# Optimization experiments

Measured on AMD Instinct MI355X. Metric: run time of the kernel, lower is better.

## Reference

```python
import jax, jax.numpy as jnp
import numpy as np

H, KV, D = 12, 4, 128  # n_head, n_kv_head, head_dim
VE_GATE_CH = 12

def _rmsnorm(x):
    eps = jnp.finfo(x.dtype).eps  # matches torch F.rms_norm default eps
    return x * jax.lax.rsqrt(jnp.mean(x * x, axis=-1, keepdims=True) + eps)

def _rope(x, cos, sin):
    d = x.shape[-1] // 2
    x1, x2 = x[..., :d], x[..., d:]
    return jnp.concatenate([x1 * cos + x2 * sin, -x1 * sin + x2 * cos], axis=-1)

def setup_inputs() -> dict:
    key = jax.random.key(0)
    ks = jax.random.split(key, 9)
    B, T, C = 2, 2048, 1536
    x = jax.random.normal(ks[0], (B, T, C), jnp.float32)
    ve = jax.random.normal(ks[1], (B, T, KV * D), jnp.float32)
    ang = jax.random.uniform(ks[2], (1, T, 1, D // 2), jnp.float32) * (2.0 * np.pi)
    cos, sin = jnp.cos(ang), jnp.sin(ang)
    Wq = jax.random.normal(ks[3], (H * D, C), jnp.float32) * 0.02
    Wk = jax.random.normal(ks[4], (KV * D, C), jnp.float32) * 0.02
    Wv = jax.random.normal(ks[5], (KV * D, C), jnp.float32) * 0.02
    Wproj = jax.random.normal(ks[6], (C, C), jnp.float32) * 0.02
    Wg = jax.random.normal(ks[7], (KV, VE_GATE_CH), jnp.float32) * 0.02
    return dict(x=x, ve=ve, cos=cos, sin=sin, Wq=Wq, Wk=Wk, Wv=Wv, Wproj=Wproj, Wg=Wg, window=1024)

def reference(x, ve, cos, sin, Wq, Wk, Wv, Wproj, Wg, window):
    B, T, C = x.shape
    q = (x @ Wq.T).reshape(B, T, H, D)
    k = (x @ Wk.T).reshape(B, T, KV, D)
    v = (x @ Wv.T).reshape(B, T, KV, D)
    # value-embedding gate: 3*sigmoid(Linear(x[..., :12])) per kv head
    gate = 3.0 * jax.nn.sigmoid(x[..., :VE_GATE_CH] @ Wg.T)  # [B,T,KV]
    v = v + gate[..., None] * ve.reshape(B, T, KV, D)
    q = _rmsnorm(_rope(q, cos, sin)) * 1.2
    k = _rmsnorm(_rope(k, cos, sin)) * 1.2
    rep = H // KV  # GQA group size
    qh = q.transpose(0, 2, 1, 3).reshape(B, KV, rep, T, D)
    kh = k.transpose(0, 2, 1, 3)  # [B,KV,T,D]
    vh = v.transpose(0, 2, 1, 3)
    scores = jnp.einsum('bgrtd,bgsd->bgrts', qh, kh) / np.sqrt(D)
    row = jnp.arange(T)[:, None]
    col = jnp.arange(T)[None, :]
    if window < 0 or window >= T:
        mask = col <= row  # pure causal
    else:
        mask = (col <= row) & (row - col <= window)  # causal sliding window
    scores = jnp.where(mask, scores, -jnp.inf)
    att = jax.nn.softmax(scores, axis=-1)
    y = jnp.einsum('bgrts,bgsd->bgrtd', att, vh)
    y = y.reshape(B, H, T, D).transpose(0, 2, 1, 3).reshape(B, T, H * D)
    return y @ Wproj.T
```

## Files before the change

kernel.cpp:

```cpp
#include <hip/hip_runtime.h>
#include <hip/hip_bf16.h>
#include <math.h>

#define B_  2
#define T_  2048
#define C_  1536
#define H_  12
#define KV_ 4
#define D_  128
#define M_  (B_*T_)
#define REP_ (H_/KV_)
#define NQKV_ 2560

typedef __bf16 bf16x8 __attribute__((ext_vector_type(8)));
typedef float  f32x4  __attribute__((ext_vector_type(4)));
typedef unsigned u32x4 __attribute__((ext_vector_type(4)));

union BCast { u32x4 u; bf16x8 b; };

__device__ inline bf16x8 ldb8(const ushort* p) {
    BCast c; c.u = *reinterpret_cast<const u32x4*>(p); return c.b;
}

__device__ inline ushort f2bf(float f) {
    union { float f; unsigned u; } v; v.f = f;
    unsigned u = v.u;
    return (ushort)((u + 0x7FFF + ((u >> 16) & 1)) >> 16);
}

__device__ inline float bf2f(ushort u) {
    union { unsigned u; float f; } v; v.u = (unsigned)u << 16;
    return v.f;
}

__device__ inline void async_copy16(const ushort* g, ushort* l) {
    __builtin_amdgcn_global_load_lds(
        (const __attribute__((address_space(1))) unsigned*)g,
        (__attribute__((address_space(3))) unsigned*)l, 16, 0, 0);
}

__device__ __host__ inline int dperm(int d) {
    return (d < 32) ? d : (d < 64 ? d + 32 : (d < 96 ? d - 32 : d));
}

template<bool BF16OUT>
__global__ __launch_bounds__(256) void gemm_bf16_bt(const ushort* __restrict__ A,
                                                    const ushort* __restrict__ Bm,
                                                    void* __restrict__ Cp,
                                                    int M, int N, int K) {
    __shared__ ushort As[128 * 32];
    __shared__ ushort Bs[128 * 32];
    const int tid  = threadIdx.x;
    const int wave = tid >> 6, lane = tid & 63;
    const int m16 = lane & 15, quad = lane >> 4;
    const int bm = blockIdx.y * 128, bn = blockIdx.x * 128;
    const int wm = (wave >> 1) * 64, wn = (wave & 1) * 64;

    const int lrow = lane >> 2;
    const int lcol = (lane & 3) * 8;
    const ushort* Ag = A  + (size_t)(bm + wave * 16 + lrow) * K + lcol;
    const ushort* Bg = Bm + (size_t)(bn + wave * 16 + lrow) * K + lcol;
    ushort* AsW0 = As + wave * 512;
    ushort* AsW1 = As + 2048 + wave * 512;
    ushort* BsW0 = Bs + wave * 512;
    ushort* BsW1 = Bs + 2048 + wave * 512;
    const size_t rowskip = (size_t)64 * K;

    f32x4 acc[4][4];
    #pragma unroll
    for (int i = 0; i < 4; i++)
        #pragma unroll
        for (int j = 0; j < 4; j++) acc[i][j] = (f32x4){0.f, 0.f, 0.f, 0.f};

    for (int k0 = 0; k0 < K; k0 += 32) {
        async_copy16(Ag + k0,           AsW0);
        async_copy16(Ag + k0 + rowskip, AsW1);
        async_copy16(Bg + k0,           BsW0);
        async_copy16(Bg + k0 + rowskip, BsW1);
        __syncthreads();

        bf16x8 af[4], bfr[4];
        #pragma unroll
        for (int i = 0; i < 4; i++)
            af[i] = ldb8(As + (wm + i * 16 + m16) * 32 + quad * 8);
        #pragma unroll
        for (int j = 0; j < 4; j++)
            bfr[j] = ldb8(Bs + (wn + j * 16 + m16) * 32 + quad * 8);
        #pragma unroll
        for (int i = 0; i < 4; i++)
            #pragma unroll
            for (int j = 0; j < 4; j++)
                acc[i][j] = __builtin_amdgcn_mfma_f32_16x16x32_bf16(af[i], bfr[j], acc[i][j], 0, 0, 0);
        __syncthreads();
    }

    #pragma unroll
    for (int i = 0; i < 4; i++) {
        #pragma unroll
        for (int reg = 0; reg < 4; reg++) {
            const int row = bm + wm + i * 16 + quad * 4 + reg;
            if constexpr (BF16OUT) {
                ushort* C = (ushort*)Cp;
                #pragma unroll
                for (int j = 0; j < 4; j++)
                    C[(size_t)row * N + bn + wn + j * 16 + m16] = f2bf(acc[i][j][reg]);
            } else {
                float* C = (float*)Cp;
                #pragma unroll
                for (int j = 0; j < 4; j++)
                    C[(size_t)row * N + bn + wn + j * 16 + m16] = acc[i][j][reg];
            }
        }
    }
}

#define KQ_ 1536
__global__ __launch_bounds__(256) void gemm_qkv(const ushort* __restrict__ A,
                                                const ushort* __restrict__ Bm,
                                                ushort* __restrict__ Qp,
                                                ushort* __restrict__ Kp,
                                                ushort* __restrict__ vbuf,
                                                const float* __restrict__ cosb,
                                                const float* __restrict__ sinb) {
    __shared__ ushort As[128 * 32];
    __shared__ ushort Bs[128 * 32];
    const int tid  = threadIdx.x;
    const int wave = tid >> 6, lane = tid & 63;
    const int m16 = lane & 15, quad = lane >> 4;
    const int bm = blockIdx.y * 128, bn = blockIdx.x * 128;
    const int wm = (wave >> 1) * 64, wn = (wave & 1) * 64;

    const int lrow = lane >> 2;
    const int lcol = (lane & 3) * 8;
    const ushort* Ag = A  + (size_t)(bm + wave * 16 + lrow) * KQ_ + lcol;
    const ushort* Bg = Bm + (size_t)(bn + wave * 16 + lrow) * KQ_ + lcol;
    ushort* AsW0 = As + wave * 512;
    ushort* AsW1 = As + 2048 + wave * 512;
    ushort* BsW0 = Bs + wave * 512;
    ushort* BsW1 = Bs + 2048 + wave * 512;
    const size_t rowskip = (size_t)64 * KQ_;

    f32x4 acc[4][4];
    #pragma unroll
    for (int i = 0; i < 4; i++)
        #pragma unroll
        for (int j = 0; j < 4; j++) acc[i][j] = (f32x4){0.f, 0.f, 0.f, 0.f};

    for (int k0 = 0; k0 < KQ_; k0 += 32) {
        async_copy16(Ag + k0,           AsW0);
        async_copy16(Ag + k0 + rowskip, AsW1);
        async_copy16(Bg + k0,           BsW0);
        async_copy16(Bg + k0 + rowskip, BsW1);
        __syncthreads();

        bf16x8 af[4], bfr[4];
        #pragma unroll
        for (int i = 0; i < 4; i++)
            af[i] = ldb8(As + (wm + i * 16 + m16) * 32 + quad * 8);
        #pragma unroll
        for (int j = 0; j < 4; j++)
            bfr[j] = ldb8(Bs + (wn + j * 16 + m16) * 32 + quad * 8);
        #pragma unroll
        for (int i = 0; i < 4; i++)
            #pragma unroll
            for (int j = 0; j < 4; j++)
                acc[i][j] = __builtin_amdgcn_mfma_f32_16x16x32_bf16(af[i], bfr[j], acc[i][j], 0, 0, 0);
        __syncthreads();
    }

    if (bn < 2048) {
        float* ssqS = (float*)As;
        float ssq[4][4];
        #pragma unroll
        for (int i = 0; i < 4; i++) {
            #pragma unroll
            for (int reg = 0; reg < 4; reg++) {
                float v = acc[i][0][reg]*acc[i][0][reg] + acc[i][1][reg]*acc[i][1][reg]
                        + acc[i][2][reg]*acc[i][2][reg] + acc[i][3][reg]*acc[i][3][reg];
                v += __shfl_xor(v, 1); v += __shfl_xor(v, 2);
                v += __shfl_xor(v, 4); v += __shfl_xor(v, 8);
                ssq[i][reg] = v;
            }
        }
        if (m16 == 0) {
            #pragma unroll
            for (int i = 0; i < 4; i++)
                #pragma unroll
                for (int reg = 0; reg < 4; reg++)
                    ssqS[(wm + i*16 + quad*4 + reg) * 2 + (wave & 1)] = ssq[i][reg];
        }
        __syncthreads();

        const bool isq = (bn < 1536);
        const float osc = isq ? (1.2f * 1.2f * 0.08838834764831845f) : 1.0f;
        const int hh  = isq ? (bn >> 7) : ((bn - 1536) >> 7);
        const int nh  = isq ? H_ : KV_;
        ushort* outp  = isq ? Qp : Kp;

        float scl[4][4];
        #pragma unroll
        for (int i = 0; i < 4; i++) {
            #pragma unroll
            for (int reg = 0; reg < 4; reg++) {
                const int r = wm + i*16 + quad*4 + reg;
                const float tot = ssqS[r*2] + ssqS[r*2 + 1];
                scl[i][reg] = rsqrtf(tot * (1.0f/128.0f) + 1.1920928955078125e-07f) * osc;
            }
        }

        #pragma unroll
        for (int i = 0; i < 4; i++) {
            #pragma unroll
            for (int reg = 0; reg < 4; reg++) {
                const int row = bm + wm + i*16 + quad*4 + reg;
                const int b = row >> 11, t = row & (T_ - 1);
                ushort* orow = outp + ((size_t)(b * nh + hh) * T_ + t) * D_;
                const float sc = scl[i][reg];
                #pragma unroll
                for (int jp = 0; jp < 2; jp++) {
                    const int ipair = (wn ? 32 : 0) + jp*16 + m16;
                    const float c = cosb[t*64 + ipair], s = sinb[t*64 + ipair];
                    const float x1 = acc[i][jp][reg], x2 = acc[i][jp+2][reg];
                    orow[wn + jp*16 + m16]       = f2bf((x1*c + x2*s) * sc);
                    orow[wn + (jp+2)*16 + m16]   = f2bf((x2*c - x1*s) * sc);
                }
            }
        }
    } else {
        const int cb = bn - 2048 + wn;
        #pragma unroll
        for (int i = 0; i < 4; i++) {
            #pragma unroll
            for (int reg = 0; reg < 4; reg++) {
                const int row = bm + wm + i*16 + quad*4 + reg;
                ushort* vr = vbuf + (size_t)row * 512 + cb + m16;
                #pragma unroll
                for (int j = 0; j < 4; j++)
                    vr[j*16] = f2bf(acc[i][j][reg]);
            }
        }
    }
}

#define SEG0 1572864
#define SEG1 2162688
#define SEG2 2359296
#define SEG3 2555904
#define SEG4 3145728
#define ROW4 384
__global__ __launch_bounds__(256) void cast_all(const float* __restrict__ x,
                                                const float* __restrict__ Wq,
                                                const float* __restrict__ Wk,
                                                const float* __restrict__ Wv,
                                                const float* __restrict__ Wp,
                                                ushort* __restrict__ xb,
                                                ushort* __restrict__ Wqkvb,
                                                ushort* __restrict__ Wpb) {
    const int i = blockIdx.x * 256 + threadIdx.x;
    float4 v; size_t dst4; ushort* dstp;
    if (i < SEG0) {
        v = ((const float4*)x)[i]; dstp = xb; dst4 = i;
    } else if (i < SEG1) {
        const int j = i - SEG0;
        const int r = j / ROW4, c4 = j - r * ROW4;
        const int d = r & 127, hh = r >> 7;
        v = ((const float4*)Wq)[j]; dstp = Wqkvb;
        dst4 = (size_t)(hh * 128 + dperm(d)) * ROW4 + c4;
    } else if (i < SEG2) {
        const int j = i - SEG1;
        const int r = j / ROW4, c4 = j - r * ROW4;
        const int d = r & 127, g = r >> 7;
        v = ((const float4*)Wk)[j]; dstp = Wqkvb;
        dst4 = (size_t)(1536 + g * 128 + dperm(d)) * ROW4 + c4;
    } else if (i < SEG3) {
        const int j = i - SEG2;
        v = ((const float4*)Wv)[j]; dstp = Wqkvb;
        dst4 = (size_t)2048 * ROW4 + j;
    } else {
        const int j = i - SEG3;
        v = ((const float4*)Wp)[j]; dstp = Wpb; dst4 = j;
    }
    ((ushort4*)dstp)[dst4] = make_ushort4(f2bf(v.x), f2bf(v.y), f2bf(v.z), f2bf(v.w));
}

__global__ __launch_bounds__(256) void gate_vt(const ushort* __restrict__ vbuf,
                                               const float* __restrict__ x,
                                               const float* __restrict__ ve,
                                               const float* __restrict__ Wg,
                                               ushort* __restrict__ Vt) {
    const int t0 = blockIdx.x * 64, g = blockIdx.y, b = blockIdx.z;
    __shared__ float gateS[64];
    __shared__ ushort tile[128][66];
    const int tid = threadIdx.x;
    if (tid < 64) {
        const float* xr = x + (size_t)(b * T_ + t0 + tid) * C_;
        float acc = 0.f;
        #pragma unroll
        for (int c = 0; c < 12; c++) acc += xr[c] * Wg[g * 12 + c];
        gateS[tid] = 3.0f / (1.0f + __expf(-acc));
    }
    __syncthreads();
    #pragma unroll
    for (int i = 0; i < 32; i++) {
        int idx = i * 256 + tid;
        int r = idx >> 7;
        int d = idx & 127;
        size_t offv = (size_t)(b * T_ + t0 + r) * 512 + g * D_ + d;
        tile[d][r] = f2bf(bf2f(vbuf[offv]) + gateS[r] * ve[offv]);
    }
    __syncthreads();
    ushort* ob = Vt + ((size_t)(b * KV_ + g) * D_) * T_ + t0;
    #pragma unroll
    for (int i = 0; i < 32; i++) {
        int idx = i * 256 + tid;
        int d = idx >> 6;
        int c = idx & 63;
        ob[(size_t)d * T_ + c] = tile[d][c];
    }
}

__global__ __launch_bounds__(256, 3) void attn_mfma(const ushort* __restrict__ Qp,
                                                    const ushort* __restrict__ Kp,
                                                    const ushort* __restrict__ Vt,
                                                    ushort* __restrict__ Y,
                                                    const int* __restrict__ wptr) {
    const int t0 = blockIdx.x * 64;
    const int h  = blockIdx.y, b = blockIdx.z;
    const int g  = h / REP_;
    const int tid  = threadIdx.x;
    const int wave = tid >> 6, lane = tid & 63;
    const int m16 = lane & 15, quad = lane >> 4;

    __shared__ ushort Ks[4 * 32 * 32];
    __shared__ ushort Vs[128 * 32];
    __shared__ ushort Pl[4][16 * 40];

    const int w = *wptr;
    const bool windowed = (w >= 0 && w < T_);
    const unsigned wu = windowed ? (unsigned)w : 0x7FFFFFFFu;
    int s_lo = 0;
    if (windowed) { s_lo = t0 - w; if (s_lo < 0) s_lo = 0; }
    const int s_hi = t0 + 63;
    const int ss0 = s_lo & ~31;
    const int tw = t0 + wave * 16;

    const ushort* qrow = Qp + ((size_t)(b * H_ + h) * T_ + tw + m16) * D_ + quad * 8;
    bf16x8 qa[4];
    #pragma unroll
    for (int kc = 0; kc < 4; kc++) qa[kc] = ldb8(qrow + kc * 32);

    const ushort* kbase = Kp + (size_t)(b * KV_ + g) * T_ * D_;
    const ushort* vbase = Vt + (size_t)(b * KV_ + g) * D_ * T_;

    const int c0 = wave, c1 = wave + 4;
    const ushort* kg0 = kbase + (size_t)((c0 & 1) * 16 + (lane >> 2)) * D_ + (c0 >> 1) * 32 + (lane & 3) * 8;
    const ushort* kg1 = kbase + (size_t)((c1 & 1) * 16 + (lane >> 2)) * D_ + (c1 >> 1) * 32 + (lane & 3) * 8;
    ushort* kl0 = Ks + c0 * 512;
    ushort* kl1 = Ks + c1 * 512;
    const ushort* vg0 = vbase + (size_t)(c0 * 16 + (lane >> 2)) * T_ + (lane & 3) * 8;
    const ushort* vg1 = vbase + (size_t)(c1 * 16 + (lane >> 2)) * T_ + (lane & 3) * 8;
    ushort* vl0 = Vs + c0 * 512;
    ushort* vl1 = Vs + c1 * 512;

    f32x4 o[8];
    #pragma unroll
    for (int dt = 0; dt < 8; dt++) o[dt] = (f32x4){0.f, 0.f, 0.f, 0.f};
    f32x4 lacc = (f32x4){0.f, 0.f, 0.f, 0.f};
    BCast onesc; onesc.u = (u32x4){0x3F803F80u, 0x3F803F80u, 0x3F803F80u, 0x3F803F80u};
    const bf16x8 ones = onesc.b;
    ushort* pw = &Pl[wave][0];

    for (int ss = ss0; ss <= s_hi; ss += 32) {
        const size_t koff = (size_t)ss * D_;
        async_copy16(kg0 + koff, kl0);
        async_copy16(kg1 + koff, kl1);
        async_copy16(vg0 + ss,   vl0);
        async_copy16(vg1 + ss,   vl1);
        __syncthreads();

        f32x4 s0 = (f32x4){0.f,0.f,0.f,0.f};
        f32x4 s1 = (f32x4){0.f,0.f,0.f,0.f};
        #pragma unroll
        for (int kc = 0; kc < 4; kc++) {
            bf16x8 kf0 = ldb8(Ks + kc * 1024 + m16 * 32 + quad * 8);
            bf16x8 kf1 = ldb8(Ks + kc * 1024 + (16 + m16) * 32 + quad * 8);
            s0 = __builtin_amdgcn_mfma_f32_16x16x32_bf16(qa[kc], kf0, s0, 0, 0, 0);
            s1 = __builtin_amdgcn_mfma_f32_16x16x32_bf16(qa[kc], kf1, s1, 0, 0, 0);
        }

        const int sA = ss + m16, sB = ss + 16 + m16;
        #pragma unroll
        for (int reg = 0; reg < 4; reg++) {
            const int t = tw + quad * 4 + reg;
            const float pa = ((unsigned)(t - sA) <= wu) ? __expf(s0[reg]) : 0.f;
            const float pb = ((unsigned)(t - sB) <= wu) ? __expf(s1[reg]) : 0.f;
            pw[(quad * 4 + reg) * 40 + m16]      = f2bf(pa);
            pw[(quad * 4 + reg) * 40 + 16 + m16] = f2bf(pb);
        }

        __builtin_amdgcn_s_waitcnt(0xc07f);
        bf16x8 pfrag = ldb8(pw + m16 * 40 + quad * 8);

        #pragma unroll
        for (int dt = 0; dt < 8; dt++) {
            bf16x8 vf = ldb8(Vs + (dt * 16 + m16) * 32 + quad * 8);
            o[dt] = __builtin_amdgcn_mfma_f32_16x16x32_bf16(pfrag, vf, o[dt], 0, 0, 0);
        }
        lacc = __builtin_amdgcn_mfma_f32_16x16x32_bf16(pfrag, ones, lacc, 0, 0, 0);
        __syncthreads();
    }

    float inv[4];
    #pragma unroll
    for (int reg = 0; reg < 4; reg++) inv[reg] = 1.0f / lacc[reg];
    ushort* yb = Y + ((size_t)(b * T_ + tw + quad * 4) * H_ + h) * D_ + m16;
    #pragma unroll
    for (int reg = 0; reg < 4; reg++)
        #pragma unroll
        for (int dt = 0; dt < 8; dt++)
            yb[(size_t)reg * H_ * D_ + dt * 16] = f2bf(o[dt][reg] * inv[reg]);
}

extern "C" void kernel_launch(void* const* d_in, const int* in_sizes, int n_in,
                              void* d_out, int out_size, void* d_ws, size_t ws_size,
                              hipStream_t stream) {
    const float* x     = (const float*)d_in[0];
    const float* ve    = (const float*)d_in[1];
    const float* cosb  = (const float*)d_in[2];
    const float* sinb  = (const float*)d_in[3];
    const float* Wq    = (const float*)d_in[4];
    const float* Wk    = (const float*)d_in[5];
    const float* Wv    = (const float*)d_in[6];
    const float* Wproj = (const float*)d_in[7];
    const float* Wg    = (const float*)d_in[8];
    const int*   wptr  = (const int*)d_in[9];
    float* out = (float*)d_out;

    ushort* xb    = (ushort*)d_ws;
    ushort* vbuf  = xb    + (size_t)M_ * C_;
    ushort* Qp    = vbuf  + (size_t)M_ * 512;
    ushort* Kp    = Qp    + (size_t)M_ * C_;
    ushort* Vt    = Kp    + (size_t)M_ * 512;
    ushort* yb16  = Vt    + (size_t)M_ * 512;
    ushort* Wqkvb = yb16  + (size_t)M_ * C_;
    ushort* Wpb   = Wqkvb + (size_t)NQKV_ * C_;

    cast_all<<<SEG4 / 256, 256, 0, stream>>>(x, Wq, Wk, Wv, Wproj, xb, Wqkvb, Wpb);

    gemm_qkv<<<dim3(NQKV_ / 128, M_ / 128), 256, 0, stream>>>(xb, Wqkvb, Qp, Kp, vbuf,
                                                              cosb, sinb);

    gate_vt<<<dim3(T_ / 64, KV_, B_), 256, 0, stream>>>(vbuf, x, ve, Wg, Vt);

    attn_mfma<<<dim3(T_ / 64, H_, B_), 256, 0, stream>>>(Qp, Kp, Vt, yb16, wptr);

    gemm_bf16_bt<false><<<dim3(C_ / 128, M_ / 128), 256, 0, stream>>>(yb16, Wpb, out, M_, C_, C_);
}
```

Baseline: 278.0 us.

## Replace QKV and output GEMMs with 256x256 double-buffered swizzled MFMA kernel

```diff
diff --git a/kernel.cpp b/kernel.cpp
--- a/kernel.cpp
+++ b/kernel.cpp
@@ -11,6 +11,8 @@
 #define M_  (B_*T_)
 #define REP_ (H_/KV_)
 #define NQKV_ 2560
+#define KK_  1536
+#define NKT_ 24
 
 typedef __bf16 bf16x8 __attribute__((ext_vector_type(8)));
 typedef float  f32x4  __attribute__((ext_vector_type(4)));
@@ -43,200 +45,221 @@
     return (d < 32) ? d : (d < 64 ? d + 32 : (d < 96 ? d - 32 : d));
 }
 
-template<bool BF16OUT>
-__global__ __launch_bounds__(256) void gemm_bf16_bt(const ushort* __restrict__ A,
-                                                    const ushort* __restrict__ Bm,
-                                                    void* __restrict__ Cp,
-                                                    int M, int N, int K) {
-    __shared__ ushort As[128 * 32];
-    __shared__ ushort Bs[128 * 32];
+__device__ __forceinline__ void phase_barrier() {
+    __builtin_amdgcn_sched_barrier(0);
+    __builtin_amdgcn_s_barrier();
+    __builtin_amdgcn_sched_barrier(0);
+}
+__device__ __forceinline__ void lgkm0_fence() {
+    __builtin_amdgcn_s_waitcnt(0xC07F);
+    __builtin_amdgcn_sched_barrier(0);
+}
+__device__ __forceinline__ bf16x8 frag_ld(const ushort* half, int row, int kbyte) {
+    const int byt = (row << 7) + (kbyte ^ ((row & 7) << 4));
+    return ldb8((const ushort*)((const char*)half + byt));
+}
+#define MFMA16(va, vb, d) d = __builtin_amdgcn_mfma_f32_16x16x32_bf16(va, vb, d, 0, 0, 0)
+
+template<int EPI>
+__global__ __launch_bounds__(512) void gemm256(const ushort* __restrict__ A,
+                                               const ushort* __restrict__ Bm,
+                                               ushort* __restrict__ Qp,
+                                               ushort* __restrict__ Kp,
+                                               ushort* __restrict__ vbuf,
+                                               float* __restrict__ Cf,
+                                               const float* __restrict__ cosb,
+                                               const float* __restrict__ sinb) {
+    __shared__ ushort lds[2][2][2][8192];
     const int tid  = threadIdx.x;
     const int wave = tid >> 6, lane = tid & 63;
     const int m16 = lane & 15, quad = lane >> 4;
-    const int bm = blockIdx.y * 128, bn = blockIdx.x * 128;
-    const int wm = (wave >> 1) * 64, wn = (wave & 1) * 64;
-
-    const int lrow = lane >> 2;
-    const int lcol = (lane & 3) * 8;
-    const ushort* Ag = A  + (size_t)(bm + wave * 16 + lrow) * K + lcol;
-    const ushort* Bg = Bm + (size_t)(bn + wave * 16 + lrow) * K + lcol;
-    ushort* AsW0 = As + wave * 512;
-    ushort* AsW1 = As + 2048 + wave * 512;
-    ushort* BsW0 = Bs + wave * 512;
-    ushort* BsW1 = Bs + 2048 + wave * 512;
-    const size_t rowskip = (size_t)64 * K;
-
-    f32x4 acc[4][4];
-    #pragma unroll
-    for (int i = 0; i < 4; i++)
+    const int WM = wave >> 2, WN = wave & 3;
+    const int bm = blockIdx.y << 8, bn = blockIdx.x << 8;
+    const int brow = (WN & 1) << 6;
+
+    const int r = tid >> 3;
+    const int slot8 = ((tid & 7) ^ (r & 7)) << 3;
+    const ushort* Ag = A  + (size_t)(bm + r) * KK_ + slot8;
+    const ushort* Bg = Bm + (size_t)(bn + r) * KK_ + slot8;
+    const size_t row64 = (size_t)64 * KK_;
+    const size_t hskip = (size_t)128 * KK_;
+
+    ushort* lbase = &lds[0][0][0][0];
+    const int wlds = wave << 9;
+
+    auto stage2 = [&](const ushort* Gp, int buf, int op, int kc) {
+        ushort* l0 = lbase + (((buf*2 + op)*2 + 0) << 13) + wlds;
+        ushort* l1 = lbase + (((buf*2 + op)*2 + 1) << 13) + wlds;
+        const ushort* g = Gp + kc;
+        async_copy16(g,                 l0);
+        async_copy16(g + row64,         l0 + 4096);
+        async_copy16(g + hskip,         l1);
+        async_copy16(g + hskip + row64, l1 + 4096);
+    };
+
+    f32x4 acc[8][4];
+    #pragma unroll
+    for (int i = 0; i < 8; i++)
         #pragma unroll
         for (int j = 0; j < 4; j++) acc[i][j] = (f32x4){0.f, 0.f, 0.f, 0.f};
 
-    for (int k0 = 0; k0 < K; k0 += 32) {
-        async_copy16(Ag + k0,           AsW0);
-        async_copy16(Ag + k0 + rowskip, AsW1);
-        async_copy16(Bg + k0,           BsW0);
-        async_copy16(Bg + k0 + rowskip, BsW1);
-        __syncthreads();
-
-        bf16x8 af[4], bfr[4];
-        #pragma unroll
-        for (int i = 0; i < 4; i++)
-            af[i] = ldb8(As + (wm + i * 16 + m16) * 32 + quad * 8);
-        #pragma unroll
-        for (int j = 0; j < 4; j++)
-            bfr[j] = ldb8(Bs + (wn + j * 16 + m16) * 32 + quad * 8);
-        #pragma unroll
-        for (int i = 0; i < 4; i++)
-            #pragma unroll
-            for (int j = 0; j < 4; j++)
-                acc[i][j] = __builtin_amdgcn_mfma_f32_16x16x32_bf16(af[i], bfr[j], acc[i][j], 0, 0, 0);
-        __syncthreads();
-    }
-
-    #pragma unroll
-    for (int i = 0; i < 4; i++) {
-        #pragma unroll
-        for (int reg = 0; reg < 4; reg++) {
-            const int row = bm + wm + i * 16 + quad * 4 + reg;
-            if constexpr (BF16OUT) {
-                ushort* C = (ushort*)Cp;
+    stage2(Bg, 0, 1, 0);  stage2(Ag, 0, 0, 0);
+    stage2(Bg, 1, 1, 64); stage2(Ag, 1, 0, 64);
+    __builtin_amdgcn_s_waitcnt(0x0F78);
+    phase_barrier();
+
+    #pragma unroll 1
+    for (int kt = 0; kt < NKT_; kt++) {
+        const int buf = kt & 1;
+        const ushort* Ah = lbase + (((buf*2 + 0)*2 + WM)        << 13);
+        const ushort* Bh = lbase + (((buf*2 + 1)*2 + (WN >> 1)) << 13);
+        const int kc2 = (kt + 2) << 6;
+        const bool stg = (kt < NKT_ - 2);
+
+        bf16x8 a[8], b0[4], b1[4];
+        #pragma unroll
+        for (int mf = 0; mf < 4; mf++) {
+            a[mf*2+0] = frag_ld(Ah, mf*16 + m16, quad*16);
+            a[mf*2+1] = frag_ld(Ah, mf*16 + m16, 64 + quad*16);
+        }
+        #pragma unroll
+        for (int nf = 0; nf < 2; nf++) {
+            b0[nf*2+0] = frag_ld(Bh, brow + nf*16 + m16, quad*16);
+            b0[nf*2+1] = frag_ld(Bh, brow + nf*16 + m16, 64 + quad*16);
+        }
+        phase_barrier();
+        lgkm0_fence();
+        __builtin_amdgcn_s_setprio(1);
+        #pragma unroll
+        for (int mf = 0; mf < 4; mf++)
+            #pragma unroll
+            for (int nf = 0; nf < 2; nf++) {
+                MFMA16(a[mf*2+0], b0[nf*2+0], acc[mf][nf]);
+                MFMA16(a[mf*2+1], b0[nf*2+1], acc[mf][nf]);
+            }
+        __builtin_amdgcn_s_setprio(0);
+        phase_barrier();
+        #pragma unroll
+        for (int nf = 0; nf < 2; nf++) {
+            b1[nf*2+0] = frag_ld(Bh, brow + 32 + nf*16 + m16, quad*16);
+            b1[nf*2+1] = frag_ld(Bh, brow + 32 + nf*16 + m16, 64 + quad*16);
+        }
+        phase_barrier();
+        lgkm0_fence();
+        __builtin_amdgcn_s_setprio(1);
+        #pragma unroll
+        for (int mf = 0; mf < 4; mf++)
+            #pragma unroll
+            for (int nf = 0; nf < 2; nf++) {
+                MFMA16(a[mf*2+0], b1[nf*2+0], acc[mf][2+nf]);
+                MFMA16(a[mf*2+1], b1[nf*2+1], acc[mf][2+nf]);
+            }
+        __builtin_amdgcn_s_setprio(0);
+        phase_barrier();
+        #pragma unroll
+        for (int mf = 0; mf < 4; mf++) {
+            a[mf*2+0] = frag_ld(Ah, 64 + mf*16 + m16, quad*16);
+            a[mf*2+1] = frag_ld(Ah, 64 + mf*16 + m16, 64 + quad*16);
+        }
+        if (stg) stage2(Bg, buf, 1, kc2);
+        phase_barrier();
+        lgkm0_fence();
+        __builtin_amdgcn_s_setprio(1);
+        #pragma unroll
+        for (int mf = 0; mf < 4; mf++)
+            #pragma unroll
+            for (int nf = 0; nf < 2; nf++) {
+                MFMA16(a[mf*2+0], b1[nf*2+0], acc[4+mf][2+nf]);
+                MFMA16(a[mf*2+1], b1[nf*2+1], acc[4+mf][2+nf]);
+            }
+        __builtin_amdgcn_s_setprio(0);
+        phase_barrier();
+        if (stg) stage2(Ag, buf, 0, kc2);
+        phase_barrier();
+        __builtin_amdgcn_s_setprio(1);
+        #pragma unroll
+        for (int mf = 0; mf < 4; mf++)
+            #pragma unroll
+            for (int nf = 0; nf < 2; nf++) {
+                MFMA16(a[mf*2+0], b0[nf*2+0], acc[4+mf][nf]);
+                MFMA16(a[mf*2+1], b0[nf*2+1], acc[4+mf][nf]);
+            }
+        __builtin_amdgcn_s_setprio(0);
+        if (stg)                 __builtin_amdgcn_s_waitcnt(0x0F78);
+        else if (kt == NKT_ - 2) __builtin_amdgcn_s_waitcnt(0x0F70);
+        phase_barrier();
+    }
+
+    if constexpr (EPI == 0) {
+        if (bn >= 2048) {
+            const int cb = bn - 2048 + WN*64;
+            #pragma unroll
+            for (int m = 0; m < 8; m++) {
+                const int rl = WM*128 + (m>>2)*64 + (m&3)*16 + quad*4;
+                #pragma unroll
+                for (int reg = 0; reg < 4; reg++) {
+                    ushort* vr = vbuf + (size_t)(bm + rl + reg) * 512 + cb + m16;
+                    #pragma unroll
+                    for (int j = 0; j < 4; j++)
+                        vr[(j>>1)*32 + (j&1)*16] = f2bf(acc[m][j][reg]);
+                }
+            }
+        } else {
+            float* ssqS = (float*)lbase;
+            #pragma unroll
+            for (int m = 0; m < 8; m++) {
+                #pragma unroll
+                for (int reg = 0; reg < 4; reg++) {
+                    float v = acc[m][0][reg]*acc[m][0][reg] + acc[m][1][reg]*acc[m][1][reg]
+                            + acc[m][2][reg]*acc[m][2][reg] + acc[m][3][reg]*acc[m][3][reg];
+                    v += __shfl_xor(v, 1); v += __shfl_xor(v, 2);
+                    v += __shfl_xor(v, 4); v += __shfl_xor(v, 8);
+                    if (m16 == 0) {
+                        const int rl = WM*128 + (m>>2)*64 + (m&3)*16 + quad*4 + reg;
+                        ssqS[rl*4 + WN] = v;
+                    }
+                }
+            }
+            __syncthreads();
+
+            const bool isq = (bn < 1536);
+            const float osc = isq ? (1.2f * 1.2f * 0.08838834764831845f) : 1.0f;
+            const int hh = (isq ? (bn >> 7) : ((bn - 1536) >> 7)) + (WN >> 1);
+            const int nh  = isq ? H_ : KV_;
+            ushort* outp  = isq ? Qp : Kp;
+
+            #pragma unroll
+            for (int m = 0; m < 8; m++) {
+                #pragma unroll
+                for (int reg = 0; reg < 4; reg++) {
+                    const int rl = WM*128 + (m>>2)*64 + (m&3)*16 + quad*4 + reg;
+                    const int row = bm + rl;
+                    const float tot = ssqS[rl*4 + (WN & ~1)] + ssqS[rl*4 + (WN | 1)];
+                    const float sc = rsqrtf(tot * (1.0f/128.0f) + 1.1920928955078125e-07f) * osc;
+                    const int b = row >> 11, t = row & (T_ - 1);
+                    ushort* orow = outp + ((size_t)(b * nh + hh) * T_ + t) * D_;
+                    #pragma unroll
+                    for (int nf = 0; nf < 2; nf++) {
+                        const int ipair = (WN & 1) * 32 + nf*16 + m16;
+                        const float c = cosb[t*64 + ipair], s = sinb[t*64 + ipair];
+                        const float x1 = acc[m][nf][reg], x2 = acc[m][2+nf][reg];
+                        const int oc = (WN & 1) * 64 + nf*16 + m16;
+                        orow[oc]      = f2bf((x1*c + x2*s) * sc);
+                        orow[oc + 32] = f2bf((x2*c - x1*s) * sc);
+                    }
+                }
+            }
+        }
+    } else {
+        #pragma unroll
+        for (int m = 0; m < 8; m++) {
+            const int rl = WM*128 + (m>>2)*64 + (m&3)*16 + quad*4;
+            #pragma unroll
+            for (int reg = 0; reg < 4; reg++) {
+                float* cr = Cf + (size_t)(bm + rl + reg) * C_ + bn + WN*64 + m16;
                 #pragma unroll
                 for (int j = 0; j < 4; j++)
-                    C[(size_t)row * N + bn + wn + j * 16 + m16] = f2bf(acc[i][j][reg]);
-            } else {
-                float* C = (float*)Cp;
-                #pragma unroll
-                for (int j = 0; j < 4; j++)
-                    C[(size_t)row * N + bn + wn + j * 16 + m16] = acc[i][j][reg];
-            }
-        }
-    }
-}
-
-#define KQ_ 1536
-__global__ __launch_bounds__(256) void gemm_qkv(const ushort* __restrict__ A,
-                                                const ushort* __restrict__ Bm,
-                                                ushort* __restrict__ Qp,
-                                                ushort* __restrict__ Kp,
-                                                ushort* __restrict__ vbuf,
-                                                const float* __restrict__ cosb,
-                                                const float* __restrict__ sinb) {
-    __shared__ ushort As[128 * 32];
-    __shared__ ushort Bs[128 * 32];
-    const int tid  = threadIdx.x;
-    const int wave = tid >> 6, lane = tid & 63;
-    const int m16 = lane & 15, quad = lane >> 4;
-    const int bm = blockIdx.y * 128, bn = blockIdx.x * 128;
-    const int wm = (wave >> 1) * 64, wn = (wave & 1) * 64;
-
-    const int lrow = lane >> 2;
-    const int lcol = (lane & 3) * 8;
-    const ushort* Ag = A  + (size_t)(bm + wave * 16 + lrow) * KQ_ + lcol;
-    const ushort* Bg = Bm + (size_t)(bn + wave * 16 + lrow) * KQ_ + lcol;
-    ushort* AsW0 = As + wave * 512;
-    ushort* AsW1 = As + 2048 + wave * 512;
-    ushort* BsW0 = Bs + wave * 512;
-    ushort* BsW1 = Bs + 2048 + wave * 512;
-    const size_t rowskip = (size_t)64 * KQ_;
-
-    f32x4 acc[4][4];
-    #pragma unroll
-    for (int i = 0; i < 4; i++)
-        #pragma unroll
-        for (int j = 0; j < 4; j++) acc[i][j] = (f32x4){0.f, 0.f, 0.f, 0.f};
-
-    for (int k0 = 0; k0 < KQ_; k0 += 32) {
-        async_copy16(Ag + k0,           AsW0);
-        async_copy16(Ag + k0 + rowskip, AsW1);
-        async_copy16(Bg + k0,           BsW0);
-        async_copy16(Bg + k0 + rowskip, BsW1);
-        __syncthreads();
-
-        bf16x8 af[4], bfr[4];
-        #pragma unroll
-        for (int i = 0; i < 4; i++)
-            af[i] = ldb8(As + (wm + i * 16 + m16) * 32 + quad * 8);
-        #pragma unroll
-        for (int j = 0; j < 4; j++)
-            bfr[j] = ldb8(Bs + (wn + j * 16 + m16) * 32 + quad * 8);
-        #pragma unroll
-        for (int i = 0; i < 4; i++)
-            #pragma unroll
-            for (int j = 0; j < 4; j++)
-                acc[i][j] = __builtin_amdgcn_mfma_f32_16x16x32_bf16(af[i], bfr[j], acc[i][j], 0, 0, 0);
-        __syncthreads();
-    }
-
-    if (bn < 2048) {
-        float* ssqS = (float*)As;
-        float ssq[4][4];
-        #pragma unroll
-        for (int i = 0; i < 4; i++) {
-            #pragma unroll
-            for (int reg = 0; reg < 4; reg++) {
-                float v = acc[i][0][reg]*acc[i][0][reg] + acc[i][1][reg]*acc[i][1][reg]
-                        + acc[i][2][reg]*acc[i][2][reg] + acc[i][3][reg]*acc[i][3][reg];
-                v += __shfl_xor(v, 1); v += __shfl_xor(v, 2);
-                v += __shfl_xor(v, 4); v += __shfl_xor(v, 8);
-                ssq[i][reg] = v;
-            }
-        }
-        if (m16 == 0) {
-            #pragma unroll
-            for (int i = 0; i < 4; i++)
-                #pragma unroll
-                for (int reg = 0; reg < 4; reg++)
-                    ssqS[(wm + i*16 + quad*4 + reg) * 2 + (wave & 1)] = ssq[i][reg];
-        }
-        __syncthreads();
-
-        const bool isq = (bn < 1536);
-        const float osc = isq ? (1.2f * 1.2f * 0.08838834764831845f) : 1.0f;
-        const int hh  = isq ? (bn >> 7) : ((bn - 1536) >> 7);
-        const int nh  = isq ? H_ : KV_;
-        ushort* outp  = isq ? Qp : Kp;
-
-        float scl[4][4];
-        #pragma unroll
-        for (int i = 0; i < 4; i++) {
-            #pragma unroll
-            for (int reg = 0; reg < 4; reg++) {
-                const int r = wm + i*16 + quad*4 + reg;
-                const float tot = ssqS[r*2] + ssqS[r*2 + 1];
-                scl[i][reg] = rsqrtf(tot * (1.0f/128.0f) + 1.1920928955078125e-07f) * osc;
-            }
-        }
-
-        #pragma unroll
-        for (int i = 0; i < 4; i++) {
-            #pragma unroll
-            for (int reg = 0; reg < 4; reg++) {
-                const int row = bm + wm + i*16 + quad*4 + reg;
-                const int b = row >> 11, t = row & (T_ - 1);
-                ushort* orow = outp + ((size_t)(b * nh + hh) * T_ + t) * D_;
-                const float sc = scl[i][reg];
-                #pragma unroll
-                for (int jp = 0; jp < 2; jp++) {
-                    const int ipair = (wn ? 32 : 0) + jp*16 + m16;
-                    const float c = cosb[t*64 + ipair], s = sinb[t*64 + ipair];
-                    const float x1 = acc[i][jp][reg], x2 = acc[i][jp+2][reg];
-                    orow[wn + jp*16 + m16]       = f2bf((x1*c + x2*s) * sc);
-                    orow[wn + (jp+2)*16 + m16]   = f2bf((x2*c - x1*s) * sc);
-                }
-            }
-        }
-    } else {
-        const int cb = bn - 2048 + wn;
-        #pragma unroll
-        for (int i = 0; i < 4; i++) {
-            #pragma unroll
-            for (int reg = 0; reg < 4; reg++) {
-                const int row = bm + wm + i*16 + quad*4 + reg;
-                ushort* vr = vbuf + (size_t)row * 512 + cb + m16;
-                #pragma unroll
-                for (int j = 0; j < 4; j++)
-                    vr[j*16] = f2bf(acc[i][j][reg]);
+                    cr[(j>>1)*32 + (j&1)*16] = acc[m][j][reg];
             }
         }
     }
@@ -447,12 +470,13 @@
 
     cast_all<<<SEG4 / 256, 256, 0, stream>>>(x, Wq, Wk, Wv, Wproj, xb, Wqkvb, Wpb);
 
-    gemm_qkv<<<dim3(NQKV_ / 128, M_ / 128), 256, 0, stream>>>(xb, Wqkvb, Qp, Kp, vbuf,
-                                                              cosb, sinb);
+    gemm256<0><<<dim3(NQKV_ / 256, M_ / 256), 512, 0, stream>>>(
+        xb, Wqkvb, Qp, Kp, vbuf, nullptr, cosb, sinb);
 
     gate_vt<<<dim3(T_ / 64, KV_, B_), 256, 0, stream>>>(vbuf, x, ve, Wg, Vt);
 
     attn_mfma<<<dim3(T_ / 64, H_, B_), 256, 0, stream>>>(Qp, Kp, Vt, yb16, wptr);
 
-    gemm_bf16_bt<false><<<dim3(C_ / 128, M_ / 128), 256, 0, stream>>>(yb16, Wpb, out, M_, C_, C_);
-}
+    gemm256<1><<<dim3(C_ / 256, M_ / 256), 512, 0, stream>>>(
+        yb16, Wpb, nullptr, nullptr, nullptr, out, nullptr, nullptr);
+}
```

Result: faster. 268.7 us (-3.3%).
